# Optimization experiments

Hardware: AMD Instinct MI355X
Metric: run time of the kernel (lower is better)

The kernel has to match this reference:

```python
import jax, jax.numpy as jnp
import numpy as np

N = 20000
E = 320000
LN_EPS = 1e-5
NEG_SLOPE = 0.2


def setup_inputs() -> dict:
    key = jax.random.key(0)
    ks = jax.random.split(key, 12)
    d = {}
    d['x'] = jax.random.normal(ks[0], (N, 512), dtype=jnp.float32)
    d['edge_index'] = jax.random.randint(ks[1], (2, E), 0, N, dtype=jnp.int64)
    s = 1.0 / np.sqrt(512.0)
    d['W1'] = jax.random.normal(ks[2], (512, 512), dtype=jnp.float32) * s
    d['a_src1'] = jax.random.normal(ks[3], (8, 64), dtype=jnp.float32) * s
    d['a_dst1'] = jax.random.normal(ks[4], (8, 64), dtype=jnp.float32) * s
    d['b1'] = jnp.zeros((512,), jnp.float32)
    d['g1'] = jnp.ones((512,), jnp.float32)
    d['beta1'] = jnp.zeros((512,), jnp.float32)
    d['W2'] = jax.random.normal(ks[5], (512, 512), dtype=jnp.float32) * s
    d['a_src2'] = jax.random.normal(ks[6], (1, 512), dtype=jnp.float32) * s
    d['a_dst2'] = jax.random.normal(ks[7], (1, 512), dtype=jnp.float32) * s
    d['b2'] = jnp.zeros((512,), jnp.float32)
    d['g2'] = jnp.ones((512,), jnp.float32)
    d['beta2'] = jnp.zeros((512,), jnp.float32)
    return d


def _segment_softmax(logits, seg, num_segments):
    # logits: [E, H]; softmax over edges sharing the same destination node
    m = jax.ops.segment_max(logits, seg, num_segments=num_segments)  # [N, H]
    e = jnp.exp(logits - m[seg])
    s = jax.ops.segment_sum(e, seg, num_segments=num_segments)  # [N, H]
    return e / s[seg]


def _gat_conv(x, src, dst, W, a_s, a_d, b, concat):
    # PyG GATConv (eval mode, self-loops already appended to src/dst)
    H, C = a_s.shape
    n = x.shape[0]
    h = (x @ W).reshape(n, H, C)                      # [N, H, C]
    alpha_s = jnp.einsum('nhc,hc->nh', h, a_s)        # [N, H]
    alpha_d = jnp.einsum('nhc,hc->nh', h, a_d)
    logits = jax.nn.leaky_relu(alpha_s[src] + alpha_d[dst], NEG_SLOPE)  # [E, H]
    alpha = _segment_softmax(logits, dst, n)          # [E, H]
    msg = h[src] * alpha[:, :, None]                  # [E, H, C]
    out = jax.ops.segment_sum(msg, dst, num_segments=n)  # [N, H, C]
    out = out.reshape(n, H * C) if concat else out.mean(axis=1)
    return out + b


def _layer_norm(x, g, beta):
    mu = jnp.mean(x, axis=-1, keepdims=True)
    var = jnp.var(x, axis=-1, keepdims=True)
    return (x - mu) * jax.lax.rsqrt(var + LN_EPS) * g + beta


def _forward(x, edge_index, W1, a_src1, a_dst1, b1, g1, beta1,
             W2, a_src2, a_dst2, b2, g2, beta2):
    n = x.shape[0]
    loops = jnp.arange(n, dtype=edge_index.dtype)
    src = jnp.concatenate([edge_index[0], loops])
    dst = jnp.concatenate([edge_index[1], loops])
    # layer 1: heads=8, concat
    x_new = _gat_conv(x, src, dst, W1, a_src1, a_dst1, b1, concat=True)
    x_new = jax.nn.elu(_layer_norm(x_new, g1, beta1))
    x = x + x_new  # 512 == 512 residual
    # layer 2: heads=1, mean (concat=False)
    x_new = _gat_conv(x, src, dst, W2, a_src2, a_dst2, b2, concat=False)
    x_new = jax.nn.elu(_layer_norm(x_new, g2, beta2))
    return x + x_new


def reference(x, edge_index, W1, a_src1, a_dst1, b1, g1, beta1,
              W2, a_src2, a_dst2, b2, g2, beta2):
    return _forward(x, edge_index, W1, a_src1, a_dst1, b1, g1, beta1,
                    W2, a_src2, a_dst2, b2, g2, beta2)
```

## Files before the change

### kernel.cpp

```cpp
#include <hip/hip_runtime.h>
#include <hip/hip_bf16.h>
#include <math.h>

#define NN 20000
#define NE 320000
#define DIM 512
#define LN_EPS 1e-5f
#define NEG_SLOPE 0.2f

typedef __attribute__((ext_vector_type(8))) short bf16x8;
typedef __attribute__((ext_vector_type(4))) float f32x4;
typedef __attribute__((ext_vector_type(4))) unsigned int u32x4;

__device__ inline void gload_lds16(const void* g, void* l) {
    __builtin_amdgcn_global_load_lds(
        (const __attribute__((address_space(1))) void*)g,
        (__attribute__((address_space(3))) void*)l, 16, 0, 0);
}

__device__ inline short f2bf(float f) {
    __hip_bfloat16 b = __float2bfloat16(f);
    return *reinterpret_cast<short*>(&b);
}

__device__ inline float bf2f(short u) {
    return __uint_as_float(((unsigned int)(unsigned short)u) << 16);
}


__global__ __launch_bounds__(1024) void scan_k(const int* __restrict__ cnt,
                                               int* __restrict__ off,
                                               int* __restrict__ cur) {
    __shared__ int s[1024];
    const int t = threadIdx.x;
    const int lo = t * 20;
    int loc[20];
    int sum = 0;
#pragma unroll
    for (int i = 0; i < 20; i++) {
        int idx = lo + i;
        int v = (idx < NN) ? cnt[idx] : 0;
        loc[i] = v; sum += v;
    }
    s[t] = sum;
    __syncthreads();
    for (int o = 1; o < 1024; o <<= 1) {
        int x = (t >= o) ? s[t - o] : 0;
        __syncthreads();
        s[t] += x;
        __syncthreads();
    }
    int run = s[t] - sum;
#pragma unroll
    for (int i = 0; i < 20; i++) {
        int idx = lo + i;
        if (idx < NN) { off[idx] = run; cur[idx] = run; run += loc[i]; }
    }
    if (t == 1023) off[NN] = s[1023];
}

__global__ void fill_k(const int* __restrict__ src, const int* __restrict__ dst,
                       int* __restrict__ cur, int* __restrict__ slot) {
    int e = blockIdx.x * blockDim.x + threadIdx.x;
    if (e < NE) {
        int d = dst[e];
        d = (d < 0) ? 0 : (d >= NN ? NN - 1 : d);
        int sv = src[e];
        sv = (sv < 0) ? 0 : (sv >= NN ? NN - 1 : sv);
        int p = atomicAdd(&cur[d], 1);
        slot[p] = sv;
    }
}

#define NB_CONV 10000
#define NB_ZERO 20
__global__ __launch_bounds__(256) void convz_k(const float* __restrict__ in,
                                               __hip_bfloat16* __restrict__ out,
                                               int* __restrict__ cnt,
                                               const float* __restrict__ W1f,
                                               const float* __restrict__ W2f,
                                               __hip_bfloat16* __restrict__ B1,
                                               __hip_bfloat16* __restrict__ B2) {
    const int b = blockIdx.x;
    if (b < NB_CONV) {
        int i = (b * 256 + threadIdx.x) * 4;
        float4 v = *(const float4*)&in[i];
        out[i + 0] = __float2bfloat16(v.x);
        out[i + 1] = __float2bfloat16(v.y);
        out[i + 2] = __float2bfloat16(v.z);
        out[i + 3] = __float2bfloat16(v.w);
    } else if (b < NB_CONV + NB_ZERO) {
        int idx = (b - NB_CONV) * 256 + threadIdx.x;
        if (idx < NN / 4) ((int4*)cnt)[idx] = make_int4(0, 0, 0, 0);
    } else {
        const int idx = b - (NB_CONV + NB_ZERO);
        const int z = idx >> 8;
        const int rem = idx & 255;
        const int bk = (rem & 15) * 32, bn = (rem >> 4) * 32;
        const float* W = z ? W2f : W1f;
        __hip_bfloat16* BT = z ? B2 : B1;
        __shared__ float tile[32][33];
        const int tx = threadIdx.x & 31, ty = threadIdx.x >> 5;
#pragma unroll
        for (int i = 0; i < 32; i += 8)
            tile[ty + i][tx] = W[(size_t)(bk + ty + i) * DIM + bn + tx];
        __syncthreads();
#pragma unroll
        for (int i = 0; i < 32; i += 8)
            BT[(size_t)(bn + ty + i) * DIM + bk + tx] = __float2bfloat16(tile[tx][ty + i]);
    }
}


template <int H>
__global__ __launch_bounds__(256) void gemm_mfma(const short* __restrict__ A,
                                                 const short* __restrict__ BT,
                                                 __hip_bfloat16* __restrict__ C,
                                                 const float* __restrict__ a_s,
                                                 const float* __restrict__ a_d,
                                                 float* __restrict__ p_as,
                                                 float* __restrict__ p_ad,
                                                 int M,
                                                 const int* __restrict__ e_dst,
                                                 int* __restrict__ cnt,
                                                 int gemmBlocks) {
    const int b = blockIdx.x;
    if (b >= gemmBlocks) {
        int e = (b - gemmBlocks) * 256 + threadIdx.x;
        if (e < NE) {
            int d = e_dst[e];
            d = (d < 0) ? 0 : (d >= NN ? NN - 1 : d);
            atomicAdd(&cnt[d], 1);
        }
        return;
    }
    const int xq = gemmBlocks >> 3, xr = gemmBlocks & 7;
    const int xcd = b & 7, pos = b >> 3;
    const int L = (xcd < xr ? xcd * (xq + 1) : xr * (xq + 1) + (xcd - xr) * xq) + pos;
    const int bx = L & 3;
    const int by = L >> 2;

    __shared__ __align__(16) short SMEM[64 * 136];
    short* As = SMEM;
    short* Bs = SMEM + 4096;
    const int t = threadIdx.x;
    const int rowBase = by * 128;
    const int colBase = bx * 128;
    const int wave = t >> 6, lane = t & 63;
    const int wr = (wave >> 1) * 64;
    const int wc = (wave & 1) * 64;
    const int quad = lane >> 4, l16 = lane & 15;

    f32x4 acc[4][4];
#pragma unroll
    for (int i = 0; i < 4; i++)
#pragma unroll
        for (int j = 0; j < 4; j++) acc[i][j] = f32x4{0.f, 0.f, 0.f, 0.f};

    const int srow = t >> 2;
    const int skof = (t & 3) * 8;
    int ar0 = rowBase + srow;       if (ar0 > M - 1) ar0 = M - 1;
    int ar1 = rowBase + 64 + srow;  if (ar1 > M - 1) ar1 = M - 1;
    const int bn0 = colBase + srow;
    const int bn1 = colBase + 64 + srow;

    for (int k0 = 0; k0 < DIM; k0 += 32) {
        gload_lds16(A + (size_t)ar0 * DIM + k0 + skof, As + t * 8);
        gload_lds16(A + (size_t)ar1 * DIM + k0 + skof, As + 2048 + t * 8);
        gload_lds16(BT + (size_t)bn0 * DIM + k0 + skof, Bs + t * 8);
        gload_lds16(BT + (size_t)bn1 * DIM + k0 + skof, Bs + 2048 + t * 8);
        __syncthreads();

        bf16x8 af[4], bfr[4];
#pragma unroll
        for (int i = 0; i < 4; i++)
            af[i] = *(const bf16x8*)&As[(wr + i * 16 + l16) * 32 + quad * 8];
#pragma unroll
        for (int j = 0; j < 4; j++)
            bfr[j] = *(const bf16x8*)&Bs[(wc + j * 16 + l16) * 32 + quad * 8];
#pragma unroll
        for (int i = 0; i < 4; i++)
#pragma unroll
            for (int j = 0; j < 4; j++)
                acc[i][j] = __builtin_amdgcn_mfma_f32_16x16x32_bf16(af[i], bfr[j], acc[i][j], 0, 0, 0);
        __syncthreads();
    }

#pragma unroll
    for (int p = 0; p < 2; p++) {
        if ((wave >> 1) == p) {
#pragma unroll
            for (int i = 0; i < 4; i++)
#pragma unroll
                for (int j = 0; j < 4; j++)
#pragma unroll
                    for (int r = 0; r < 4; r++)
                        SMEM[(i * 16 + quad * 4 + r) * 136 + wc + j * 16 + l16] =
                            f2bf(acc[i][j][r]);
        }
        __syncthreads();
#pragma unroll
        for (int k = 0; k < 4; k++) {
            const int row = k * 16 + (t >> 4);
            const int col = (t & 15) * 8;
            const int gr = rowBase + p * 64 + row;
            if (gr < M) {
                bf16x8 vv = *(const bf16x8*)&SMEM[row * 136 + col];
                *(bf16x8*)&C[(size_t)gr * DIM + colBase + col] = vv;
            }
        }
        __syncthreads();
    }

    const int slab = 2 * bx + (wave & 1);
    const int cb = (H == 8) ? slab * 64 : (colBase + wc);
    float asc[4], adc[4];
#pragma unroll
    for (int j = 0; j < 4; j++) {
        asc[j] = a_s[cb + j * 16 + l16];
        adc[j] = a_d[cb + j * 16 + l16];
    }
#pragma unroll
    for (int i = 0; i < 4; i++) {
#pragma unroll
        for (int r = 0; r < 4; r++) {
            float vs = acc[i][0][r] * asc[0] + acc[i][1][r] * asc[1] +
                       acc[i][2][r] * asc[2] + acc[i][3][r] * asc[3];
            float vd = acc[i][0][r] * adc[0] + acc[i][1][r] * adc[1] +
                       acc[i][2][r] * adc[2] + acc[i][3][r] * adc[3];
#pragma unroll
            for (int o = 8; o; o >>= 1) { vs += __shfl_down(vs, o); vd += __shfl_down(vd, o); }
            if (l16 == 0) {
                const int row = rowBase + wr + i * 16 + quad * 4 + r;
                if (row < M) {
                    if (H == 8) {
                        p_as[(size_t)row * 8 + slab] = vs;
                        p_ad[(size_t)row * 8 + slab] = vd;
                    } else {
                        atomicAdd(&p_as[row], vs);
                        atomicAdd(&p_ad[row], vd);
                    }
                }
            }
        }
    }
}


template <int H>
__global__ __launch_bounds__(256) void agg_k(const __hip_bfloat16* __restrict__ h,
                                             const float* __restrict__ alp_s,
                                             const float* __restrict__ alp_d,
                                             const int* __restrict__ off,
                                             const int* __restrict__ slot,
                                             const float* __restrict__ bias,
                                             const float* __restrict__ gamma,
                                             const float* __restrict__ beta,
                                             const __hip_bfloat16* x_resb,
                                             float* x_out,
                                             __hip_bfloat16* x_out_b,
                                             float* __restrict__ zs,
                                             float* __restrict__ zd) {
    if (H == 8 && threadIdx.x < 4) {
        const int zi = blockIdx.x * 4 + threadIdx.x;
        if (zi < NN) { zs[zi] = 0.f; zd[zi] = 0.f; }
    }
    const int wid = threadIdx.x >> 6;
    const int lane = threadIdx.x & 63;
    const int n = blockIdx.x * 4 + wid;
    const int head = (H == 8) ? (lane >> 3) : 0;

    const int o0 = off[n];
    const int deg = off[n + 1] - o0;
    const int total = deg + 1;

    const float ad = (H == 8) ? alp_d[(size_t)n * 8 + head] : alp_d[n];

    int v = 0x7fffffff;
    if (lane < total && lane < 64) v = (lane < deg) ? slot[o0 + lane] : n;
#pragma unroll
    for (int k = 2; k <= 64; k <<= 1) {
#pragma unroll
        for (int j = k >> 1; j > 0; j >>= 1) {
            int o = __shfl_xor(v, j);
            bool takeMin = (((lane & k) == 0) == ((lane & j) == 0));
            v = takeMin ? min(v, o) : max(v, o);
        }
    }
    const int nsort = (total < 64) ? total : 64;

    float acc[8];
#pragma unroll
    for (int r = 0; r < 8; r++) acc[r] = 0.f;
    float ld = 0.f;
    const unsigned short* hu = (const unsigned short*)h;

    auto zcomp = [&](int s) -> float {
        float z = ((H == 8) ? alp_s[(size_t)s * 8 + head] : alp_s[s]) + ad;
        return (z >= 0.f) ? z : NEG_SLOPE * z;
    };
    auto fmarow = [&](const u32x4& rv, float p) {
#pragma unroll
        for (int q = 0; q < 4; q++) {
            unsigned int u = rv[q];
            acc[2 * q]     += p * __uint_as_float(u << 16);
            acc[2 * q + 1] += p * __uint_as_float(u & 0xffff0000u);
        }
    };

    int e = 0;
    for (; e + 4 <= nsort; e += 4) {
        const int s0 = __shfl(v, e), s1 = __shfl(v, e + 1);
        const int s2 = __shfl(v, e + 2), s3 = __shfl(v, e + 3);
        const u32x4 r0 = *(const u32x4*)(hu + (size_t)s0 * DIM + lane * 8);
        const u32x4 r1 = *(const u32x4*)(hu + (size_t)s1 * DIM + lane * 8);
        const u32x4 r2 = *(const u32x4*)(hu + (size_t)s2 * DIM + lane * 8);
        const u32x4 r3 = *(const u32x4*)(hu + (size_t)s3 * DIM + lane * 8);
        const float z0 = zcomp(s0), z1 = zcomp(s1), z2 = zcomp(s2), z3 = zcomp(s3);
        const float p0 = __expf(z0), p1 = __expf(z1), p2 = __expf(z2), p3 = __expf(z3);
        ld += p0; fmarow(r0, p0);
        ld += p1; fmarow(r1, p1);
        ld += p2; fmarow(r2, p2);
        ld += p3; fmarow(r3, p3);
    }
    for (; e < nsort; e++) {
        const int s = __shfl(v, e);
        const u32x4 rv = *(const u32x4*)(hu + (size_t)s * DIM + lane * 8);
        const float p = __expf(zcomp(s));
        ld += p; fmarow(rv, p);
    }
    for (int e2 = 64; e2 < total; e2++) {
        const int s = (e2 < deg) ? slot[o0 + e2] : n;
        const u32x4 rv = *(const u32x4*)(hu + (size_t)s * DIM + lane * 8);
        const float p = __expf(zcomp(s));
        ld += p; fmarow(rv, p);
    }

    const float inv = 1.f / ld;
    const int c0 = lane * 8;
    const float4 ba = *(const float4*)&bias[c0];
    const float4 bb = *(const float4*)&bias[c0 + 4];
    float xn[8];
    xn[0] = acc[0] * inv + ba.x; xn[1] = acc[1] * inv + ba.y;
    xn[2] = acc[2] * inv + ba.z; xn[3] = acc[3] * inv + ba.w;
    xn[4] = acc[4] * inv + bb.x; xn[5] = acc[5] * inv + bb.y;
    xn[6] = acc[6] * inv + bb.z; xn[7] = acc[7] * inv + bb.w;

    float s1 = 0.f, s2 = 0.f;
#pragma unroll
    for (int r = 0; r < 8; r++) { s1 += xn[r]; s2 += xn[r] * xn[r]; }
#pragma unroll
    for (int o = 32; o; o >>= 1) { s1 += __shfl_xor(s1, o); s2 += __shfl_xor(s2, o); }
    const float mu = s1 * (1.f / DIM);
    const float rs = rsqrtf(s2 * (1.f / DIM) - mu * mu + LN_EPS);

    const float4 ga = *(const float4*)&gamma[c0];
    const float4 gb = *(const float4*)&gamma[c0 + 4];
    const float4 ea = *(const float4*)&beta[c0];
    const float4 eb = *(const float4*)&beta[c0 + 4];
    const bf16x8 xrv = *(const bf16x8*)&x_resb[(size_t)n * DIM + c0];
    const float gv[8] = {ga.x, ga.y, ga.z, ga.w, gb.x, gb.y, gb.z, gb.w};
    const float ev[8] = {ea.x, ea.y, ea.z, ea.w, eb.x, eb.y, eb.z, eb.w};

    float out[8];
#pragma unroll
    for (int r = 0; r < 8; r++) {
        float y = (xn[r] - mu) * rs * gv[r] + ev[r];
        y = (y > 0.f) ? y : expm1f(y);
        out[r] = bf2f(xrv[r]) + y;
    }
    if (x_out) {
        *(float4*)&x_out[(size_t)n * DIM + c0]     = make_float4(out[0], out[1], out[2], out[3]);
        *(float4*)&x_out[(size_t)n * DIM + c0 + 4] = make_float4(out[4], out[5], out[6], out[7]);
    }
    if (x_out_b) {
        __hip_bfloat16 tb[8];
#pragma unroll
        for (int r = 0; r < 8; r++) tb[r] = __float2bfloat16(out[r]);
        *(bf16x8*)&x_out_b[(size_t)n * DIM + c0] = *(bf16x8*)tb;
    }
}


extern "C" void kernel_launch(void* const* d_in, const int* in_sizes, int n_in,
                              void* d_out, int out_size, void* d_ws, size_t ws_size,
                              hipStream_t stream) {
    const float* x = (const float*)d_in[0];
    const int* ei = (const int*)d_in[1];
    const float* W1 = (const float*)d_in[2];
    const float* as1 = (const float*)d_in[3];
    const float* ad1 = (const float*)d_in[4];
    const float* b1 = (const float*)d_in[5];
    const float* g1 = (const float*)d_in[6];
    const float* be1 = (const float*)d_in[7];
    const float* W2 = (const float*)d_in[8];
    const float* as2 = (const float*)d_in[9];
    const float* ad2 = (const float*)d_in[10];
    const float* b2 = (const float*)d_in[11];
    const float* g2 = (const float*)d_in[12];
    const float* be2 = (const float*)d_in[13];
    float* out = (float*)d_out;

    char* ws = (char*)d_ws;
    size_t o = 0;
    auto alloc = [&](size_t bytes) { size_t r = o; o += (bytes + 255) & ~(size_t)255; return r; };
    int* p_cnt = (int*)(ws + alloc((size_t)NN * 4));
    int* p_off = (int*)(ws + alloc((size_t)(NN + 1) * 4));
    int* p_cur = (int*)(ws + alloc((size_t)NN * 4));
    int* p_slot = (int*)(ws + alloc((size_t)NE * 4));
    __hip_bfloat16* p_hb = (__hip_bfloat16*)(ws + alloc((size_t)NN * DIM * 2));
    __hip_bfloat16* p_xb = (__hip_bfloat16*)(ws + alloc((size_t)NN * DIM * 2));
    __hip_bfloat16* p_bt1 = (__hip_bfloat16*)(ws + alloc((size_t)DIM * DIM * 2));
    __hip_bfloat16* p_bt2 = (__hip_bfloat16*)(ws + alloc((size_t)DIM * DIM * 2));
    float* p_as = (float*)(ws + alloc((size_t)NN * 8 * 4));
    float* p_ad = (float*)(ws + alloc((size_t)NN * 8 * 4));
    float* p_as2 = (float*)(ws + alloc((size_t)NN * 4));
    float* p_ad2 = (float*)(ws + alloc((size_t)NN * 4));

    const int* e_src = ei;
    const int* e_dst = ei + NE;

    const int GB = 4 * ((NN + 127) / 128);
    const int CB = (NE + 255) / 256;

    convz_k<<<NB_CONV + NB_ZERO + 512, 256, 0, stream>>>(x, p_xb, p_cnt, W1, W2, p_bt1, p_bt2);
    gemm_mfma<8><<<GB + CB, 256, 0, stream>>>((const short*)p_xb, (const short*)p_bt1, p_hb,
                                              as1, ad1, p_as, p_ad, NN, e_dst, p_cnt, GB);
    scan_k<<<1, 1024, 0, stream>>>(p_cnt, p_off, p_cur);
    fill_k<<<CB, 256, 0, stream>>>(e_src, e_dst, p_cur, p_slot);
    agg_k<8><<<NN / 4, 256, 0, stream>>>(p_hb, p_as, p_ad, p_off, p_slot, b1, g1, be1,
                                         p_xb, nullptr, p_xb, p_as2, p_ad2);
    gemm_mfma<1><<<GB, 256, 0, stream>>>((const short*)p_xb, (const short*)p_bt2, p_hb,
                                         as2, ad2, p_as2, p_ad2, NN, nullptr, nullptr, GB);
    agg_k<1><<<NN / 4, 256, 0, stream>>>(p_hb, p_as2, p_ad2, p_off, p_slot, b2, g2, be2,
                                         p_xb, out, nullptr, nullptr, nullptr);
}
```

Measured before the change: 309.2 us.

## Add weight-stationary GEMM for layer 2 with full B slab in LDS

Replaces the layer-2 GEMM with a persistent-style kernel of 512 blocks. Each block loads a 128x512 slab of the transposed weight into LDS once, using an XOR swizzle, and then processes up to two 128-row tiles. The A fragments are read directly from global memory with no LDS staging. The aim is to cut repeated B loads and per-tile LDS staging, at the cost of 128KB of LDS per block (one block per CU) and uncached global A reads.

```diff
diff --git a/kernel.cpp b/kernel.cpp
--- a/kernel.cpp
+++ b/kernel.cpp
@@ -247,6 +247,115 @@
 }
 
 
+__global__ __launch_bounds__(256) void gemm_ws1(const short* __restrict__ A,
+                                                const short* __restrict__ BT,
+                                                __hip_bfloat16* __restrict__ C,
+                                                const float* __restrict__ a_s,
+                                                const float* __restrict__ a_d,
+                                                float* __restrict__ p_as,
+                                                float* __restrict__ p_ad,
+                                                int M) {
+    __shared__ __align__(16) short Bs[128 * 512];
+    const int t = threadIdx.x;
+    const int b = blockIdx.x;
+    const int L = (b & 7) * 64 + (b >> 3);
+    const int slabIdx = L & 3;
+    const int q = L >> 2;
+    const int colBase = slabIdx * 128;
+    const int wave = t >> 6, lane = t & 63;
+    const int wr = (wave >> 1) * 64;
+    const int wc = (wave & 1) * 64;
+    const int quad = lane >> 4, l16 = lane & 15;
+
+#pragma unroll
+    for (int i = 0; i < 32; i++) {
+        const int s = t + 256 * i;
+        const int c = s >> 6;
+        const int k8 = (s & 63) * 8;
+        const int ksrc = k8 ^ ((c & 7) * 8);
+        gload_lds16(BT + (size_t)(colBase + c) * DIM + ksrc, Bs + (size_t)s * 8);
+    }
+    __syncthreads();
+
+    const int swz = (l16 & 7) * 8;
+
+    const int ng = (q + 128 < (M + 127) / 128) ? 2 : 1;
+    for (int gi = 0; gi < ng; gi++) {
+        const int g = (gi == 0) ? q : q + 128;
+        const int rowBase = g * 128;
+
+        f32x4 acc[4][4];
+#pragma unroll
+        for (int i = 0; i < 4; i++)
+#pragma unroll
+            for (int j = 0; j < 4; j++) acc[i][j] = f32x4{0.f, 0.f, 0.f, 0.f};
+
+        int arow[4];
+#pragma unroll
+        for (int i = 0; i < 4; i++) {
+            int r = rowBase + wr + i * 16 + l16;
+            arow[i] = (r > M - 1) ? (M - 1) : r;
+        }
+
+#pragma unroll 4
+        for (int k0 = 0; k0 < DIM; k0 += 32) {
+            bf16x8 af[4], bfr[4];
+#pragma unroll
+            for (int i = 0; i < 4; i++)
+                af[i] = *(const bf16x8*)&A[(size_t)arow[i] * DIM + k0 + quad * 8];
+#pragma unroll
+            for (int j = 0; j < 4; j++)
+                bfr[j] = *(const bf16x8*)&Bs[(wc + j * 16 + l16) * 512 + ((k0 + quad * 8) ^ swz)];
+#pragma unroll
+            for (int i = 0; i < 4; i++)
+#pragma unroll
+                for (int j = 0; j < 4; j++)
+                    acc[i][j] = __builtin_amdgcn_mfma_f32_16x16x32_bf16(af[i], bfr[j], acc[i][j], 0, 0, 0);
+        }
+
+#pragma unroll
+        for (int i = 0; i < 4; i++) {
+#pragma unroll
+            for (int r = 0; r < 4; r++) {
+                const int row = rowBase + wr + i * 16 + quad * 4 + r;
+                if (row < M) {
+#pragma unroll
+                    for (int j = 0; j < 4; j++)
+                        *(short*)&C[(size_t)row * DIM + colBase + wc + j * 16 + l16] =
+                            f2bf(acc[i][j][r]);
+                }
+            }
+        }
+
+        float asc[4], adc[4];
+#pragma unroll
+        for (int j = 0; j < 4; j++) {
+            asc[j] = a_s[colBase + wc + j * 16 + l16];
+            adc[j] = a_d[colBase + wc + j * 16 + l16];
+        }
+#pragma unroll
+        for (int i = 0; i < 4; i++) {
+#pragma unroll
+            for (int r = 0; r < 4; r++) {
+                float vs = acc[i][0][r] * asc[0] + acc[i][1][r] * asc[1] +
+                           acc[i][2][r] * asc[2] + acc[i][3][r] * asc[3];
+                float vd = acc[i][0][r] * adc[0] + acc[i][1][r] * adc[1] +
+                           acc[i][2][r] * adc[2] + acc[i][3][r] * adc[3];
+#pragma unroll
+                for (int o = 8; o; o >>= 1) { vs += __shfl_down(vs, o); vd += __shfl_down(vd, o); }
+                if (l16 == 0) {
+                    const int row = rowBase + wr + i * 16 + quad * 4 + r;
+                    if (row < M) {
+                        atomicAdd(&p_as[row], vs);
+                        atomicAdd(&p_ad[row], vd);
+                    }
+                }
+            }
+        }
+    }
+}
+
+
 template <int H>
 __global__ __launch_bounds__(256) void agg_k(const __hip_bfloat16* __restrict__ h,
                                              const float* __restrict__ alp_s,
@@ -430,8 +539,8 @@
     fill_k<<<CB, 256, 0, stream>>>(e_src, e_dst, p_cur, p_slot);
     agg_k<8><<<NN / 4, 256, 0, stream>>>(p_hb, p_as, p_ad, p_off, p_slot, b1, g1, be1,
                                          p_xb, nullptr, p_xb, p_as2, p_ad2);
-    gemm_mfma<1><<<GB, 256, 0, stream>>>((const short*)p_xb, (const short*)p_bt2, p_hb,
-                                         as2, ad2, p_as2, p_ad2, NN, nullptr, nullptr, GB);
+    gemm_ws1<<<512, 256, 0, stream>>>((const short*)p_xb, (const short*)p_bt2, p_hb,
+                                      as2, ad2, p_as2, p_ad2, NN);
     agg_k<1><<<NN / 4, 256, 0, stream>>>(p_hb, p_as2, p_ad2, p_off, p_slot, b2, g2, be2,
                                          p_xb, out, nullptr, nullptr, nullptr);
 }
```

Result: slower. 343.0 us (+10.9%).

## Replace single-block prefix scan with wave-level atomic bucket allocation

Applied to the files above, without the earlier changes.

The single 1024-thread block exclusive scan over node degrees becomes a many-block kernel. Each wave computes a local prefix with shuffles and reserves a contiguous range by atomically adding to a global counter, so CSR offsets are no longer in node order. Degrees are now read directly from the count array instead of off[n+1]-off[n]. This removes a serial single-block launch and its many barriers, but makes the edge layout depend on atomic ordering and can hurt locality of the slot array.

```diff
diff --git a/kernel.cpp b/kernel.cpp
--- a/kernel.cpp
+++ b/kernel.cpp
@@ -28,35 +28,26 @@
 }
 
 
-__global__ __launch_bounds__(1024) void scan_k(const int* __restrict__ cnt,
-                                               int* __restrict__ off,
-                                               int* __restrict__ cur) {
-    __shared__ int s[1024];
-    const int t = threadIdx.x;
-    const int lo = t * 20;
-    int loc[20];
-    int sum = 0;
-#pragma unroll
-    for (int i = 0; i < 20; i++) {
-        int idx = lo + i;
-        int v = (idx < NN) ? cnt[idx] : 0;
-        loc[i] = v; sum += v;
-    }
-    s[t] = sum;
-    __syncthreads();
-    for (int o = 1; o < 1024; o <<= 1) {
-        int x = (t >= o) ? s[t - o] : 0;
-        __syncthreads();
-        s[t] += x;
-        __syncthreads();
-    }
-    int run = s[t] - sum;
-#pragma unroll
-    for (int i = 0; i < 20; i++) {
-        int idx = lo + i;
-        if (idx < NN) { off[idx] = run; cur[idx] = run; run += loc[i]; }
-    }
-    if (t == 1023) off[NN] = s[1023];
+__global__ void alloc_k(const int* __restrict__ cnt, int* __restrict__ off,
+                        int* __restrict__ cur, int* __restrict__ gtot) {
+    const int n = blockIdx.x * blockDim.x + threadIdx.x;
+    const int lane = threadIdx.x & 63;
+    int c = (n < NN) ? cnt[n] : 0;
+    int pre = c;
+#pragma unroll
+    for (int o = 1; o < 64; o <<= 1) {
+        int t = __shfl_up(pre, o);
+        if (lane >= o) pre += t;
+    }
+    int wtot = __shfl(pre, 63);
+    int base = 0;
+    if (lane == 63) base = atomicAdd(gtot, wtot);
+    base = __shfl(base, 63);
+    if (n < NN) {
+        int o0 = base + pre - c;
+        off[n] = o0;
+        cur[n] = o0;
+    }
 }
 
 __global__ void fill_k(const int* __restrict__ src, const int* __restrict__ dst,
@@ -80,7 +71,8 @@
                                                const float* __restrict__ W1f,
                                                const float* __restrict__ W2f,
                                                __hip_bfloat16* __restrict__ B1,
-                                               __hip_bfloat16* __restrict__ B2) {
+                                               __hip_bfloat16* __restrict__ B2,
+                                               int* __restrict__ gtot) {
     const int b = blockIdx.x;
     if (b < NB_CONV) {
         int i = (b * 256 + threadIdx.x) * 4;
@@ -92,6 +84,7 @@
     } else if (b < NB_CONV + NB_ZERO) {
         int idx = (b - NB_CONV) * 256 + threadIdx.x;
         if (idx < NN / 4) ((int4*)cnt)[idx] = make_int4(0, 0, 0, 0);
+        if (idx == 0) *gtot = 0;
     } else {
         const int idx = b - (NB_CONV + NB_ZERO);
         const int z = idx >> 8;
@@ -252,6 +245,7 @@
                                              const float* __restrict__ alp_s,
                                              const float* __restrict__ alp_d,
                                              const int* __restrict__ off,
+                                             const int* __restrict__ degc,
                                              const int* __restrict__ slot,
                                              const float* __restrict__ bias,
                                              const float* __restrict__ gamma,
@@ -271,7 +265,7 @@
     const int head = (H == 8) ? (lane >> 3) : 0;
 
     const int o0 = off[n];
-    const int deg = off[n + 1] - o0;
+    const int deg = degc[n];
     const int total = deg + 1;
 
     const float ad = (H == 8) ? alp_d[(size_t)n * 8 + head] : alp_d[n];
@@ -416,6 +410,7 @@
     float* p_ad = (float*)(ws + alloc((size_t)NN * 8 * 4));
     float* p_as2 = (float*)(ws + alloc((size_t)NN * 4));
     float* p_ad2 = (float*)(ws + alloc((size_t)NN * 4));
+    int* p_gtot = (int*)(ws + alloc(256));
 
     const int* e_src = ei;
     const int* e_dst = ei + NE;
@@ -423,15 +418,16 @@
     const int GB = 4 * ((NN + 127) / 128);
     const int CB = (NE + 255) / 256;
 
-    convz_k<<<NB_CONV + NB_ZERO + 512, 256, 0, stream>>>(x, p_xb, p_cnt, W1, W2, p_bt1, p_bt2);
+    convz_k<<<NB_CONV + NB_ZERO + 512, 256, 0, stream>>>(x, p_xb, p_cnt, W1, W2, p_bt1, p_bt2,
+                                                         p_gtot);
     gemm_mfma<8><<<GB + CB, 256, 0, stream>>>((const short*)p_xb, (const short*)p_bt1, p_hb,
                                               as1, ad1, p_as, p_ad, NN, e_dst, p_cnt, GB);
-    scan_k<<<1, 1024, 0, stream>>>(p_cnt, p_off, p_cur);
+    alloc_k<<<(NN + 255) / 256, 256, 0, stream>>>(p_cnt, p_off, p_cur, p_gtot);
     fill_k<<<CB, 256, 0, stream>>>(e_src, e_dst, p_cur, p_slot);
-    agg_k<8><<<NN / 4, 256, 0, stream>>>(p_hb, p_as, p_ad, p_off, p_slot, b1, g1, be1,
+    agg_k<8><<<NN / 4, 256, 0, stream>>>(p_hb, p_as, p_ad, p_off, p_cnt, p_slot, b1, g1, be1,
                                          p_xb, nullptr, p_xb, p_as2, p_ad2);
     gemm_mfma<1><<<GB, 256, 0, stream>>>((const short*)p_xb, (const short*)p_bt2, p_hb,
                                          as2, ad2, p_as2, p_ad2, NN, nullptr, nullptr, GB);
-    agg_k<1><<<NN / 4, 256, 0, stream>>>(p_hb, p_as2, p_ad2, p_off, p_slot, b2, g2, be2,
+    agg_k<1><<<NN / 4, 256, 0, stream>>>(p_hb, p_as2, p_ad2, p_off, p_cnt, p_slot, b2, g2, be2,
                                          p_xb, out, nullptr, nullptr, nullptr);
 }
```

New measurement: 288.0 us. 1.07x faster.
